# Kernel tuning notes

Measured on AMD Instinct MI355X. Metric: run time of the kernel, lower is better.

## Reference

```python
import jax, jax.numpy as jnp
import numpy as np
import math

SPARSITY = 0.95


def _linear(x, W, b):
    # torch nn.Linear: y = x @ W.T + b, W is [out, in]
    return jnp.einsum('bsd,od->bso', x, W) + b


def setup_inputs() -> dict:
    key = jax.random.key(0)
    ks = jax.random.split(key, 11)
    B, S, D = 2, 4096, 512
    std = 1.0 / math.sqrt(D)
    inp = {
        'x': jax.random.normal(ks[0], (B, S, D), dtype=jnp.float32),
        'mask_rand': jax.random.uniform(ks[1], (B, S, S), dtype=jnp.float32),
        'Wq': jax.random.normal(ks[2], (D, D), dtype=jnp.float32) * std,
        'bq': jax.random.normal(ks[3], (D,), dtype=jnp.float32) * std,
        'Wk': jax.random.normal(ks[4], (D, D), dtype=jnp.float32) * std,
        'bk': jax.random.normal(ks[5], (D,), dtype=jnp.float32) * std,
        'Wv': jax.random.normal(ks[6], (D, D), dtype=jnp.float32) * std,
        'bv': jax.random.normal(ks[7], (D,), dtype=jnp.float32) * std,
        'Wo': jax.random.normal(ks[8], (D, D), dtype=jnp.float32) * std,
        'bo': jax.random.normal(ks[9], (D,), dtype=jnp.float32) * std,
    }
    return inp


def reference(x, mask_rand, Wq, bq, Wk, bk, Wv, bv, Wo, bo):
    B, S, D = x.shape
    Q = _linear(x, Wq, bq)
    K = _linear(x, Wk, bk)
    V = _linear(x, Wv, bv)
    scores = jnp.einsum('bqd,bkd->bqk', Q, K) / jnp.sqrt(jnp.asarray(D, x.dtype))
    keep = mask_rand > SPARSITY  # random sparsity mask
    sparse_scores = jnp.where(keep, scores, -jnp.inf)
    attn = jax.nn.softmax(sparse_scores, axis=-1)
    attn_out = jnp.einsum('bqk,bkd->bqd', attn, V)
    # faithful to torch: transpose(1,2).contiguous().view(B, S, D)
    attn_out = jnp.swapaxes(attn_out, 1, 2).reshape(B, S, D)
    return _linear(attn_out, Wo, bo)
```

## Files before the change

kernel.cpp:

```cpp
#include <hip/hip_runtime.h>
#include <hip/hip_bf16.h>
#include <math.h>

typedef __bf16 bf16_t;
typedef __attribute__((ext_vector_type(8))) __bf16 bf16x8;
typedef __attribute__((ext_vector_type(4))) float f32x4;

constexpr int B_ = 2, S_ = 4096, D_ = 512;
constexpr int BS_ = B_ * S_;
constexpr int GRID_ = 512;
constexpr int NT_ = 256;
constexpr long QKV_E  = (long)BS_ * D_;
constexpr long W_E    = (long)D_ * D_;
constexpr long MASK_N = (long)BS_ * S_;
constexpr long CVT_UNITS  = (QKV_E + 4 * W_E) / 4;
constexpr long PACK_UNITS = MASK_N / 16;
constexpr float SCALE_ = 0.044194173824159216f;

__device__ __forceinline__ void load16_lds(const bf16_t* g, bf16_t* l) {
    __builtin_amdgcn_global_load_lds(
        (const __attribute__((address_space(1))) void*)g,
        (__attribute__((address_space(3))) void*)l, 16, 0, 0);
}

__device__ __forceinline__ void dev_cvt(long u,
    const float* x, const float* Wq, const float* Wk, const float* Wv,
    const float* Wo, bf16_t* dst)
{
    const long i = u * 4;
    const float* src; long o;
    if (i < QKV_E) { src = x; o = i; }
    else {
        const long j = i - QKV_E;
        const int w = (int)(j >> 18);
        o = j & (W_E - 1);
        src = (w == 0) ? Wq : (w == 1) ? Wk : (w == 2) ? Wv : Wo;
    }
    const float4 v = *(const float4*)(src + o);
    bf16_t out[4] = {(bf16_t)v.x, (bf16_t)v.y, (bf16_t)v.z, (bf16_t)v.w};
    *(uint2*)(dst + i) = *(uint2*)out;
}

__device__ __forceinline__ void dev_pack(long u,
    const float* mask, unsigned char* bm)
{
    const long i = u * 16;
    unsigned char o[16];
#pragma unroll
    for (int c = 0; c < 4; c++) {
        const float4 v = *(const float4*)(mask + i + c * 4);
        o[c * 4 + 0] = v.x > 0.95f;
        o[c * 4 + 1] = v.y > 0.95f;
        o[c * 4 + 2] = v.z > 0.95f;
        o[c * 4 + 3] = v.w > 0.95f;
    }
    *(uint4*)(bm + i) = *(uint4*)o;
}

__device__ __forceinline__ void kloop64(
    const bf16_t* At, const bf16_t* Bt, long ldA, long ldB, int kSteps,
    bf16_t* As, bf16_t* Bs, int tid, int wr, int wc, int quad, int r16,
    f32x4 (&acc)[4][4])
{
    const int srow = tid >> 3;
    const int cg = ((tid & 7) ^ (srow & 7)) * 8;
    const bf16_t* gA = At + (long)srow * ldA + cg;
    const bf16_t* gB = Bt + (long)srow * ldB + cg;
    bf16_t* lA = As + tid * 8;
    bf16_t* lB = Bs + tid * 8;

    for (int s = 0; s < kSteps; s++) {
        const int k0 = s * 64;
#pragma unroll
        for (int rr = 0; rr < 4; rr++) {
            load16_lds(gA + (long)rr * 32 * ldA + k0, lA + rr * 2048);
            load16_lds(gB + (long)rr * 32 * ldB + k0, lB + rr * 2048);
        }
        __syncthreads();
#pragma unroll
        for (int kh = 0; kh < 2; kh++) {
            bf16x8 af[4], bfr[4];
#pragma unroll
            for (int i = 0; i < 4; i++) {
                const int row = wr * 64 + i * 16 + r16;
                af[i] = *(const bf16x8*)(As + row * 64 +
                        (((kh << 2) + quad) ^ (row & 7)) * 8);
            }
#pragma unroll
            for (int j = 0; j < 4; j++) {
                const int row = wc * 64 + j * 16 + r16;
                bfr[j] = *(const bf16x8*)(Bs + row * 64 +
                        (((kh << 2) + quad) ^ (row & 7)) * 8);
            }
#pragma unroll
            for (int i = 0; i < 4; i++)
#pragma unroll
                for (int j = 0; j < 4; j++)
                    acc[i][j] = __builtin_amdgcn_mfma_f32_16x16x32_bf16(
                        af[i], bfr[j], acc[i][j], 0, 0, 0);
        }
        __syncthreads();
    }
}

__device__ __forceinline__ void dev_qkv_tile(int t,
    const bf16_t* Xc, const bf16_t* Wqc, const bf16_t* Wkc, const bf16_t* Wvc,
    const float* bq, const float* bk, const float* bv,
    bf16_t* Q, bf16_t* Kp, bf16_t* VT, char* smem, int tid)
{
    constexpr int K = 512;
    const int sel = t >> 8;
    const int tt  = t & 255;

    bf16_t* As = (bf16_t*)smem;
    bf16_t* Bs = As + 128 * 64;
    const int wave = tid >> 6, lane = tid & 63;
    const int quad = lane >> 4, r16 = lane & 15;
    const int wr = wave >> 1, wc = wave & 1;

    f32x4 acc[4][4] = {};

    if (sel < 2) {
        const int m0 = (tt >> 2) * 128;
        const int n0 = (tt & 3) * 128;
        const bf16_t* Bw = sel ? Wkc : Wqc;
        const float* bias = sel ? bk : bq;
        bf16_t* C = sel ? Kp : Q;
        kloop64(Xc + (long)m0 * K, Bw + (long)n0 * K, K, K, K / 64,
                As, Bs, tid, wr, wc, quad, r16, acc);
#pragma unroll
        for (int i = 0; i < 4; i++)
#pragma unroll
            for (int j = 0; j < 4; j++) {
                const int gn = n0 + wc * 64 + j * 16 + r16;
                const float bval = bias[gn];
#pragma unroll
                for (int reg = 0; reg < 4; reg++) {
                    const int gm = m0 + wr * 64 + i * 16 + quad * 4 + reg;
                    C[(long)gm * 512 + gn] = (bf16_t)(acc[i][j][reg] + bval);
                }
            }
    } else {
        const int m0 = (tt & 3) * 128;
        const int n0 = (tt >> 2) * 128;
        kloop64(Wvc + (long)m0 * K, Xc + (long)n0 * K, K, K, K / 64,
                As, Bs, tid, wr, wc, quad, r16, acc);
#pragma unroll
        for (int i = 0; i < 4; i++)
#pragma unroll
            for (int j = 0; j < 4; j++) {
                const int gn = n0 + wc * 64 + j * 16 + r16;
                const int b = gn >> 12, q = gn & 4095;
#pragma unroll
                for (int reg = 0; reg < 4; reg++) {
                    const int gm = m0 + wr * 64 + i * 16 + quad * 4 + reg;
                    VT[(long)b * D_ * S_ + (long)gm * S_ + q] =
                        (bf16_t)(acc[i][j][reg] + bv[gm]);
                }
            }
    }
}

__device__ __forceinline__ void dev_scores_tile(int t,
    const bf16_t* Q, const bf16_t* Kp, const unsigned char* bmask,
    bf16_t* SC, float* rowsum, char* smem, int tid)
{
    constexpr int S = S_, K = D_;
    const int x = t & 31;
    const int y = (t >> 5) & 31;
    const int b = t >> 10;
    const int m0 = y * 128, n0 = x * 128;

    bf16_t* As = (bf16_t*)smem;
    bf16_t* Bs = As + 128 * 64;
    const int wave = tid >> 6, lane = tid & 63;
    const int quad = lane >> 4, r16 = lane & 15;
    const int wr = wave >> 1, wc = wave & 1;

    f32x4 acc[4][4] = {};
    kloop64(Q + (long)b * S * K + (long)m0 * K,
            Kp + (long)b * S * K + (long)n0 * K, K, K, K / 64,
            As, Bs, tid, wr, wc, quad, r16, acc);

    float* wlds = (float*)smem + wave * 1088;
    const int erow = lane >> 2;
    const int ecg  = lane & 3;
    const long mbase = (long)b * S * S;

#pragma unroll
    for (int i = 0; i < 4; i++) {
#pragma unroll
        for (int j = 0; j < 4; j++)
#pragma unroll
            for (int reg = 0; reg < 4; reg++)
                wlds[(quad * 4 + reg) * 68 + j * 16 + r16] = acc[i][j][reg];
        __syncthreads();

        float v[16];
#pragma unroll
        for (int c = 0; c < 4; c++) {
            const float4 tv = *(const float4*)(wlds + erow * 68 + ecg * 16 + c * 4);
            v[c * 4 + 0] = tv.x; v[c * 4 + 1] = tv.y;
            v[c * 4 + 2] = tv.z; v[c * 4 + 3] = tv.w;
        }

        const int gm = m0 + wr * 64 + i * 16 + erow;
        const int gn = n0 + wc * 64 + ecg * 16;

        const uint4 mb = *(const uint4*)(bmask + mbase + (long)gm * S + gn);
        const unsigned char* mk = (const unsigned char*)&mb;
        float e[16];
#pragma unroll
        for (int tt = 0; tt < 16; tt++)
            e[tt] = mk[tt] ? __expf(v[tt] * SCALE_) : 0.f;

        bf16x8 o0, o1;
        float rsum = 0.f;
#pragma unroll
        for (int tt = 0; tt < 8; tt++) {
            rsum += e[tt] + e[tt + 8];
            o0[tt] = (bf16_t)e[tt];
            o1[tt] = (bf16_t)e[tt + 8];
        }
        bf16_t* cp = SC + mbase + (long)gm * S + gn;
        *(bf16x8*)cp       = o0;
        *(bf16x8*)(cp + 8) = o1;

        rsum += __shfl_xor(rsum, 1, 64);
        rsum += __shfl_xor(rsum, 2, 64);
        if (ecg == 0) atomicAdd(&rowsum[b * S + gm], rsum);
        __syncthreads();
    }
}

__device__ __forceinline__ void dev_pv_tile(int t,
    const bf16_t* VT, const bf16_t* SC, const float* rowsum,
    bf16_t* part, char* smem, int tid)
{
    constexpr int S = S_, D = D_;
    constexpr int KC = S / 2;
    const int x = t & 31;
    const int y = (t >> 5) & 3;
    const int z = t >> 7;
    const int b = z >> 1, ks = z & 1;
    const int m0 = y * 128, n0 = x * 128;
    const int kbeg = ks * KC;

    bf16_t* As = (bf16_t*)smem;
    bf16_t* Bs = As + 128 * 64;
    const int wave = tid >> 6, lane = tid & 63;
    const int quad = lane >> 4, r16 = lane & 15;
    const int wr = wave >> 1, wc = wave & 1;

    f32x4 acc[4][4] = {};
    kloop64(VT + (long)b * D * S + (long)m0 * S + kbeg,
            SC + (long)b * S * S + (long)n0 * S + kbeg, S, S, KC / 64,
            As, Bs, tid, wr, wc, quad, r16, acc);

    const long obase = ((long)ks * B_ + b) * (long)D * S;
#pragma unroll
    for (int i = 0; i < 4; i++)
#pragma unroll
        for (int j = 0; j < 4; j++) {
            const int gn = n0 + wc * 64 + j * 16 + r16;
            const float inv = 1.f / rowsum[b * S + gn];
#pragma unroll
            for (int reg = 0; reg < 4; reg++) {
                const int gm = m0 + wr * 64 + i * 16 + quad * 4 + reg;
                part[obase + (long)gm * S + gn] = (bf16_t)(acc[i][j][reg] * inv);
            }
        }
}

__device__ __forceinline__ void dev_out_tile(int t,
    const bf16_t* part, const bf16_t* Woc, const float* bo, float* C,
    char* smem, int tid)
{
    constexpr int N = 512, K = 512;
    const int m0 = (t >> 2) * 128, n0 = (t & 3) * 128;

    bf16_t* As = (bf16_t*)smem;
    bf16_t* Bs = As + 128 * 64;
    const int wave = tid >> 6, lane = tid & 63;
    const int quad = lane >> 4, r16 = lane & 15;
    const int wr = wave >> 1, wc = wave & 1;

    const int srow = tid >> 3;
    const int cg = ((tid & 7) ^ (srow & 7)) * 8;
    const bf16_t* gA0 = part + (long)(m0 + srow) * K + cg;
    const bf16_t* gA1 = gA0 + QKV_E;
    const bf16_t* gB  = Woc + (long)(n0 + srow) * K + cg;
    bf16_t* lA = As + tid * 8;
    bf16_t* lB = Bs + tid * 8;

    f32x4 acc[4][4] = {};

    for (int s = 0; s < K / 64; s++) {
        const int k0 = s * 64;
#pragma unroll
        for (int rr = 0; rr < 4; rr++) {
            const bf16x8 a0 = *(const bf16x8*)(gA0 + (long)rr * 32 * K + k0);
            const bf16x8 a1 = *(const bf16x8*)(gA1 + (long)rr * 32 * K + k0);
            bf16x8 sm;
#pragma unroll
            for (int e = 0; e < 8; e++)
                sm[e] = (bf16_t)((float)a0[e] + (float)a1[e]);
            *(bf16x8*)(lA + rr * 2048) = sm;
            load16_lds(gB + (long)rr * 32 * K + k0, lB + rr * 2048);
        }
        __syncthreads();
#pragma unroll
        for (int kh = 0; kh < 2; kh++) {
            bf16x8 af[4], bfr[4];
#pragma unroll
            for (int i = 0; i < 4; i++) {
                const int row = wr * 64 + i * 16 + r16;
                af[i] = *(const bf16x8*)(As + row * 64 +
                        (((kh << 2) + quad) ^ (row & 7)) * 8);
            }
#pragma unroll
            for (int j = 0; j < 4; j++) {
                const int row = wc * 64 + j * 16 + r16;
                bfr[j] = *(const bf16x8*)(Bs + row * 64 +
                        (((kh << 2) + quad) ^ (row & 7)) * 8);
            }
#pragma unroll
            for (int i = 0; i < 4; i++)
#pragma unroll
                for (int j = 0; j < 4; j++)
                    acc[i][j] = __builtin_amdgcn_mfma_f32_16x16x32_bf16(
                        af[i], bfr[j], acc[i][j], 0, 0, 0);
        }
        __syncthreads();
    }

#pragma unroll
    for (int i = 0; i < 4; i++)
#pragma unroll
        for (int j = 0; j < 4; j++) {
            const int gn = n0 + wc * 64 + j * 16 + r16;
            const float bval = bo[gn];
#pragma unroll
            for (int reg = 0; reg < 4; reg++) {
                const int gm = m0 + wr * 64 + i * 16 + quad * 4 + reg;
                C[(long)gm * N + gn] = acc[i][j][reg] + bval;
            }
        }
}

__global__ __launch_bounds__(256) void k_s1(
    const float* x, const float* mask, const float* Wq, const float* Wk,
    const float* Wv, const float* Wo, bf16_t* Xc, unsigned char* bmask,
    float* rowsum)
{
    const long gtid = (long)blockIdx.x * NT_ + threadIdx.x;
    for (long u = gtid; u < CVT_UNITS; u += (long)GRID_ * NT_)
        dev_cvt(u, x, Wq, Wk, Wv, Wo, Xc);
    for (long u = gtid; u < PACK_UNITS; u += (long)GRID_ * NT_)
        dev_pack(u, mask, bmask);
    if (gtid < BS_ / 4) {
        const float4 z = {0.f, 0.f, 0.f, 0.f};
        *(float4*)(rowsum + gtid * 4) = z;
    }
}

__global__ __launch_bounds__(256) void k_s2(
    const bf16_t* Xc, const float* bq, const float* bk, const float* bv,
    bf16_t* Q, bf16_t* Kp, bf16_t* VT)
{
    __shared__ char smem[32768];
    const bf16_t* Wqc = Xc + QKV_E;
    for (int t = blockIdx.x; t < 768; t += GRID_)
        dev_qkv_tile(t, Xc, Wqc, Wqc + W_E, Wqc + 2 * W_E,
                     bq, bk, bv, Q, Kp, VT, smem, threadIdx.x);
}

__global__ __launch_bounds__(256) void k_s3(
    const bf16_t* Q, const bf16_t* Kp, const unsigned char* bmask,
    bf16_t* SC, float* rowsum)
{
    __shared__ char smem[32768];
    for (int t = blockIdx.x; t < 2048; t += GRID_)
        dev_scores_tile(t, Q, Kp, bmask, SC, rowsum, smem, threadIdx.x);
}

__global__ __launch_bounds__(256) void k_s4(
    const bf16_t* VT, const bf16_t* SC, const float* rowsum, bf16_t* part)
{
    __shared__ char smem[32768];
    dev_pv_tile(blockIdx.x, VT, SC, rowsum, part, smem, threadIdx.x);
}

__global__ __launch_bounds__(256) void k_s6(
    const bf16_t* part, const bf16_t* Xc, const float* bo, float* C)
{
    __shared__ char smem[32768];
    const bf16_t* Woc = Xc + QKV_E + 3 * W_E;
    dev_out_tile(blockIdx.x, part, Woc, bo, C, smem, threadIdx.x);
}

extern "C" void kernel_launch(void* const* d_in, const int* in_sizes, int n_in,
                              void* d_out, int out_size, void* d_ws, size_t ws_size,
                              hipStream_t stream)
{
    const float* x    = (const float*)d_in[0];
    const float* mask = (const float*)d_in[1];
    const float* Wq   = (const float*)d_in[2];
    const float* bq   = (const float*)d_in[3];
    const float* Wk   = (const float*)d_in[4];
    const float* bk   = (const float*)d_in[5];
    const float* Wv   = (const float*)d_in[6];
    const float* bv   = (const float*)d_in[7];
    const float* Wo   = (const float*)d_in[8];
    const float* bo   = (const float*)d_in[9];
    float* outp = (float*)d_out;

    char* ws = (char*)d_ws;
    bf16_t* SC = (bf16_t*)ws;   ws += (long)BS_ * S_ * 2;
    bf16_t* VT = (bf16_t*)ws;   ws += QKV_E * 2;
    bf16_t* Q  = (bf16_t*)ws;   ws += QKV_E * 2;
    bf16_t* Kp = (bf16_t*)ws;   ws += QKV_E * 2;
    bf16_t* Xc = (bf16_t*)ws;   ws += (QKV_E + 4 * W_E) * 2;
    float* rowsum = (float*)ws; ws += (long)BS_ * 4;
    unsigned char* bmask = (unsigned char*)ws;
    bf16_t* part = (bf16_t*)ws;

    dim3 blk(NT_);
    k_s1<<<dim3(GRID_), blk, 0, stream>>>(x, mask, Wq, Wk, Wv, Wo,
                                          Xc, bmask, rowsum);
    k_s2<<<dim3(GRID_), blk, 0, stream>>>(Xc, bq, bk, bv, Q, Kp, VT);
    k_s3<<<dim3(GRID_), blk, 0, stream>>>(Q, Kp, bmask, SC, rowsum);
    k_s4<<<dim3(GRID_), blk, 0, stream>>>(VT, SC, rowsum, part);
    k_s6<<<dim3(256), blk, 0, stream>>>(part, Xc, bo, outp);
}
```

Baseline: 370.8 us.

## Fuse all stages into one persistent kernel with grid barriers, read float mask directly

```diff
diff --git a/kernel.cpp b/kernel.cpp
--- a/kernel.cpp
+++ b/kernel.cpp
@@ -12,15 +12,30 @@
 constexpr int NT_ = 256;
 constexpr long QKV_E  = (long)BS_ * D_;
 constexpr long W_E    = (long)D_ * D_;
-constexpr long MASK_N = (long)BS_ * S_;
-constexpr long CVT_UNITS  = (QKV_E + 4 * W_E) / 4;
-constexpr long PACK_UNITS = MASK_N / 16;
+constexpr long CVT_UNITS = (QKV_E + 4 * W_E) / 4;
 constexpr float SCALE_ = 0.044194173824159216f;
 
 __device__ __forceinline__ void load16_lds(const bf16_t* g, bf16_t* l) {
     __builtin_amdgcn_global_load_lds(
         (const __attribute__((address_space(1))) void*)g,
         (__attribute__((address_space(3))) void*)l, 16, 0, 0);
+}
+
+__device__ __forceinline__ void gbar(unsigned* bar, int idx) {
+    __syncthreads();
+    if (threadIdx.x == 0) {
+        unsigned* c = bar + idx * 32;
+        __threadfence();
+        __hip_atomic_fetch_add(c, 1u, __ATOMIC_RELEASE, __HIP_MEMORY_SCOPE_AGENT);
+        long guard = 0;
+        while (__hip_atomic_load(c, __ATOMIC_ACQUIRE, __HIP_MEMORY_SCOPE_AGENT)
+               < (unsigned)GRID_) {
+            if (++guard > (1L << 21)) break;
+            __builtin_amdgcn_s_sleep(8);
+        }
+        __threadfence();
+    }
+    __syncthreads();
 }
 
 __device__ __forceinline__ void dev_cvt(long u,
@@ -41,22 +56,6 @@
     *(uint2*)(dst + i) = *(uint2*)out;
 }
 
-__device__ __forceinline__ void dev_pack(long u,
-    const float* mask, unsigned char* bm)
-{
-    const long i = u * 16;
-    unsigned char o[16];
-#pragma unroll
-    for (int c = 0; c < 4; c++) {
-        const float4 v = *(const float4*)(mask + i + c * 4);
-        o[c * 4 + 0] = v.x > 0.95f;
-        o[c * 4 + 1] = v.y > 0.95f;
-        o[c * 4 + 2] = v.z > 0.95f;
-        o[c * 4 + 3] = v.w > 0.95f;
-    }
-    *(uint4*)(bm + i) = *(uint4*)o;
-}
-
 __device__ __forceinline__ void kloop64(
     const bf16_t* At, const bf16_t* Bt, long ldA, long ldB, int kSteps,
     bf16_t* As, bf16_t* Bs, int tid, int wr, int wc, int quad, int r16,
@@ -162,7 +161,7 @@
 }
 
 __device__ __forceinline__ void dev_scores_tile(int t,
-    const bf16_t* Q, const bf16_t* Kp, const unsigned char* bmask,
+    const bf16_t* Q, const bf16_t* Kp, const float* mask,
     bf16_t* SC, float* rowsum, char* smem, int tid)
 {
     constexpr int S = S_, K = D_;
@@ -207,12 +206,16 @@
         const int gm = m0 + wr * 64 + i * 16 + erow;
         const int gn = n0 + wc * 64 + ecg * 16;
 
-        const uint4 mb = *(const uint4*)(bmask + mbase + (long)gm * S + gn);
-        const unsigned char* mk = (const unsigned char*)&mb;
+        const float* mp = mask + mbase + (long)gm * S + gn;
         float e[16];
 #pragma unroll
-        for (int tt = 0; tt < 16; tt++)
-            e[tt] = mk[tt] ? __expf(v[tt] * SCALE_) : 0.f;
+        for (int c = 0; c < 4; c++) {
+            const float4 mk = *(const float4*)(mp + c * 4);
+            e[c * 4 + 0] = (mk.x > 0.95f) ? __expf(v[c * 4 + 0] * SCALE_) : 0.f;
+            e[c * 4 + 1] = (mk.y > 0.95f) ? __expf(v[c * 4 + 1] * SCALE_) : 0.f;
+            e[c * 4 + 2] = (mk.z > 0.95f) ? __expf(v[c * 4 + 2] * SCALE_) : 0.f;
+            e[c * 4 + 3] = (mk.w > 0.95f) ? __expf(v[c * 4 + 3] * SCALE_) : 0.f;
+        }
 
         bf16x8 o0, o1;
         float rsum = 0.f;
@@ -348,55 +351,53 @@
         }
 }
 
-__global__ __launch_bounds__(256) void k_s1(
-    const float* x, const float* mask, const float* Wq, const float* Wk,
-    const float* Wv, const float* Wo, bf16_t* Xc, unsigned char* bmask,
-    float* rowsum)
-{
-    const long gtid = (long)blockIdx.x * NT_ + threadIdx.x;
+__global__ __launch_bounds__(256) void k_init(unsigned* bar)
+{
+    if (threadIdx.x < 128) bar[threadIdx.x] = 0u;
+}
+
+__global__ __launch_bounds__(256, 2) void mega(
+    const float* __restrict__ x, const float* __restrict__ mask,
+    const float* __restrict__ Wq, const float* __restrict__ bq,
+    const float* __restrict__ Wk, const float* __restrict__ bk,
+    const float* __restrict__ Wv, const float* __restrict__ bv,
+    const float* __restrict__ Wo, const float* __restrict__ bo,
+    float* __restrict__ outp,
+    bf16_t* Xc, bf16_t* Q, bf16_t* Kp, bf16_t* VT,
+    bf16_t* SC, bf16_t* part, float* rowsum, unsigned* bar)
+{
+    __shared__ char smem[32768];
+    const int tid = threadIdx.x;
+    const int bid = blockIdx.x;
+    const long gtid = (long)bid * NT_ + tid;
+
+    const bf16_t* Wqc = Xc + QKV_E;
+    const bf16_t* Wkc = Wqc + W_E;
+    const bf16_t* Wvc = Wkc + W_E;
+    const bf16_t* Woc = Wvc + W_E;
+
     for (long u = gtid; u < CVT_UNITS; u += (long)GRID_ * NT_)
         dev_cvt(u, x, Wq, Wk, Wv, Wo, Xc);
-    for (long u = gtid; u < PACK_UNITS; u += (long)GRID_ * NT_)
-        dev_pack(u, mask, bmask);
     if (gtid < BS_ / 4) {
         const float4 z = {0.f, 0.f, 0.f, 0.f};
         *(float4*)(rowsum + gtid * 4) = z;
     }
-}
-
-__global__ __launch_bounds__(256) void k_s2(
-    const bf16_t* Xc, const float* bq, const float* bk, const float* bv,
-    bf16_t* Q, bf16_t* Kp, bf16_t* VT)
-{
-    __shared__ char smem[32768];
-    const bf16_t* Wqc = Xc + QKV_E;
-    for (int t = blockIdx.x; t < 768; t += GRID_)
-        dev_qkv_tile(t, Xc, Wqc, Wqc + W_E, Wqc + 2 * W_E,
-                     bq, bk, bv, Q, Kp, VT, smem, threadIdx.x);
-}
-
-__global__ __launch_bounds__(256) void k_s3(
-    const bf16_t* Q, const bf16_t* Kp, const unsigned char* bmask,
-    bf16_t* SC, float* rowsum)
-{
-    __shared__ char smem[32768];
-    for (int t = blockIdx.x; t < 2048; t += GRID_)
-        dev_scores_tile(t, Q, Kp, bmask, SC, rowsum, smem, threadIdx.x);
-}
-
-__global__ __launch_bounds__(256) void k_s4(
-    const bf16_t* VT, const bf16_t* SC, const float* rowsum, bf16_t* part)
-{
-    __shared__ char smem[32768];
-    dev_pv_tile(blockIdx.x, VT, SC, rowsum, part, smem, threadIdx.x);
-}
-
-__global__ __launch_bounds__(256) void k_s6(
-    const bf16_t* part, const bf16_t* Xc, const float* bo, float* C)
-{
-    __shared__ char smem[32768];
-    const bf16_t* Woc = Xc + QKV_E + 3 * W_E;
-    dev_out_tile(blockIdx.x, part, Woc, bo, C, smem, threadIdx.x);
+    gbar(bar, 0);
+
+    for (int t = bid; t < 768; t += GRID_)
+        dev_qkv_tile(t, Xc, Wqc, Wkc, Wvc, bq, bk, bv, Q, Kp, VT, smem, tid);
+    gbar(bar, 1);
+
+    for (int t = bid; t < 2048; t += GRID_)
+        dev_scores_tile(t, Q, Kp, mask, SC, rowsum, smem, tid);
+    gbar(bar, 2);
+
+    for (int t = bid; t < 512; t += GRID_)
+        dev_pv_tile(t, VT, SC, rowsum, part, smem, tid);
+    gbar(bar, 3);
+
+    for (int t = bid; t < 256; t += GRID_)
+        dev_out_tile(t, part, Woc, bo, outp, smem, tid);
 }
 
 extern "C" void kernel_launch(void* const* d_in, const int* in_sizes, int n_in,
@@ -421,15 +422,13 @@
     bf16_t* Q  = (bf16_t*)ws;   ws += QKV_E * 2;
     bf16_t* Kp = (bf16_t*)ws;   ws += QKV_E * 2;
     bf16_t* Xc = (bf16_t*)ws;   ws += (QKV_E + 4 * W_E) * 2;
+    bf16_t* part = (bf16_t*)ws; ws += 2 * QKV_E * 2;
     float* rowsum = (float*)ws; ws += (long)BS_ * 4;
-    unsigned char* bmask = (unsigned char*)ws;
-    bf16_t* part = (bf16_t*)ws;
+    unsigned* bar = (unsigned*)ws;
 
     dim3 blk(NT_);
-    k_s1<<<dim3(GRID_), blk, 0, stream>>>(x, mask, Wq, Wk, Wv, Wo,
-                                          Xc, bmask, rowsum);
-    k_s2<<<dim3(GRID_), blk, 0, stream>>>(Xc, bq, bk, bv, Q, Kp, VT);
-    k_s3<<<dim3(GRID_), blk, 0, stream>>>(Q, Kp, bmask, SC, rowsum);
-    k_s4<<<dim3(GRID_), blk, 0, stream>>>(VT, SC, rowsum, part);
-    k_s6<<<dim3(256), blk, 0, stream>>>(part, Xc, bo, outp);
-}
+    k_init<<<dim3(1), blk, 0, stream>>>(bar);
+    mega<<<dim3(GRID_), blk, 0, stream>>>(
+        x, mask, Wq, bq, Wk, bk, Wv, bv, Wo, bo, outp,
+        Xc, Q, Kp, VT, SC, part, rowsum, bar);
+}
```

Measured after the change: 740.9 us. 2x slower.
